# Performance work log

Measured on AMD Instinct MI355X. Metric: run time of the kernel, lower is better.

The kernel has to match this reference:

```python
import jax, jax.numpy as jnp
import numpy as np

B, S, H = 64, 2048, 512


def setup_inputs() -> dict:
    key = jax.random.key(0)
    ks = jax.random.split(key, 7)
    sc = 1.0 / np.sqrt(H)
    return {
        "encoder_outputs": jax.random.normal(ks[0], (B, S, H), dtype=jnp.float32),
        "hidden": jax.random.normal(ks[1], (B, H), dtype=jnp.float32),
        "W1": jax.random.uniform(ks[2], (H, H), jnp.float32, -sc, sc),
        "b1": jax.random.uniform(ks[3], (H,), jnp.float32, -sc, sc),
        "W2": jax.random.uniform(ks[4], (H, H), jnp.float32, -sc, sc),
        "b2": jax.random.uniform(ks[5], (H,), jnp.float32, -sc, sc),
        "V": jax.random.uniform(ks[6], (H, 1), jnp.float32, -sc, sc),
        "bV": jnp.zeros((1,), dtype=jnp.float32),
    }


def reference(encoder_outputs, hidden, W1, b1, W2, b2, V, bV):
    # score: tanh(W1(enc) + W2(hidden)) ; hidden broadcast over seq dim (no repeat materialized)
    proj_enc = jnp.einsum("bsh,hk->bsk", encoder_outputs, W1) + b1          # [B,S,H]
    proj_hid = (hidden @ W2 + b2)[:, None, :]                                 # [B,1,H]
    score = jnp.tanh(proj_enc + proj_hid)                                     # [B,S,H]
    logits = jnp.einsum("bsh,hk->bsk", score, V) + bV                        # [B,S,1]
    attention_weights = jax.nn.softmax(logits, axis=1)                        # softmax over seq
    context = jnp.sum(attention_weights * encoder_outputs, axis=1)            # [B,H]
    return context, attention_weights
```

## Files before the change

### kernel.cpp

```cpp
#include <hip/hip_runtime.h>
#include <hip/hip_bf16.h>
#include <cstdint>
#include <cstddef>

#define B_ 64
#define S_ 2048
#define H_ 512

typedef __bf16 bf16x8 __attribute__((ext_vector_type(8)));
typedef float  f32x4  __attribute__((ext_vector_type(4)));

__device__ __forceinline__ float fast_tanh(float x) {
    float e = __expf(2.0f * x);
    return 1.0f - __fdividef(2.0f, e + 1.0f);
}

__global__ __launch_bounds__(256) void prep_kernel(const float* __restrict__ W1,
                                                   unsigned short* __restrict__ Wt,
                                                   const float* __restrict__ hidden,
                                                   const float* __restrict__ W2,
                                                   const float* __restrict__ b1,
                                                   const float* __restrict__ b2,
                                                   float* __restrict__ cvals) {
    if (blockIdx.x < 256) {
        __shared__ float tile[32][33];
        int tn = blockIdx.x >> 4;
        int tk = blockIdx.x & 15;
        int lx = threadIdx.x & 31;
        int ly = threadIdx.x >> 5;
#pragma unroll
        for (int i = 0; i < 4; ++i) {
            int k = tk * 32 + ly + i * 8;
            tile[ly + i * 8][lx] = W1[k * H_ + tn * 32 + lx];
        }
        __syncthreads();
#pragma unroll
        for (int i = 0; i < 4; ++i) {
            int n = tn * 32 + ly + i * 8;
            float v = tile[lx][ly + i * 8];
            __bf16 bv = (__bf16)v;
            Wt[(size_t)n * H_ + tk * 32 + lx] = *(unsigned short*)&bv;
        }
    } else {
        int blk = blockIdx.x - 256;
        int b = blk >> 1;
        int h = (blk & 1) * 256 + threadIdx.x;
        float acc = b1[h] + b2[h];
        const float* hp = hidden + b * H_;
        const float* wp = W2 + h;
#pragma unroll 16
        for (int k = 0; k < H_; ++k) acc = fmaf(hp[k], wp[(size_t)k * H_], acc);
        cvals[b * H_ + h] = acc;
    }
}

__global__ __launch_bounds__(256, 4) void score_kernel(const float* __restrict__ enc,
                                                       const unsigned short* __restrict__ Wt,
                                                       const float* __restrict__ cvals,
                                                       const float* __restrict__ Vp,
                                                       float* __restrict__ logits) {
    __shared__ __align__(16) unsigned short As[128 * 64];
    __shared__ __align__(16) unsigned short Bs[128 * 64];

    int orig = blockIdx.x;
    int wg   = (orig & 7) * 512 + (orig >> 3);
    int b     = wg >> 6;
    int stile = (wg >> 2) & 15;
    int ntile = wg & 3;

    int tid  = threadIdx.x;
    int wid  = tid >> 6;
    int lane = tid & 63;
    int wm = wid >> 1, wn = wid & 1;
    int rsel = lane & 15;
    int g    = lane >> 4;

    f32x4 acc[4][4];
#pragma unroll
    for (int m = 0; m < 4; ++m)
#pragma unroll
        for (int n = 0; n < 4; ++n) acc[m][n] = (f32x4){0.f, 0.f, 0.f, 0.f};

    const float*          Abase = enc + ((size_t)(b * S_ + stile * 128)) * H_;
    const unsigned short* Bbase = Wt + ((size_t)(ntile * 128)) * H_;

    int srow = tid >> 1;
    int shalf = (tid & 1);
    int c0 = shalf * 2;

    float4 ra[4];
    bf16x8 rb[2];

    auto swz = [&](int row, int nbc) -> int {
        return row * 64 + ((nbc ^ (row & 7)) << 3);
    };

    auto loadAB = [&](int kt) {
        const float* ap = Abase + (size_t)srow * H_ + kt * 32 + shalf * 16;
        ra[0] = *(const float4*)(ap);
        ra[1] = *(const float4*)(ap + 4);
        ra[2] = *(const float4*)(ap + 8);
        ra[3] = *(const float4*)(ap + 12);
        const unsigned short* bp = Bbase + (size_t)srow * H_ + kt * 32 + shalf * 16;
        rb[0] = *(const bf16x8*)(bp);
        rb[1] = *(const bf16x8*)(bp + 8);
    };
    auto writeAB = [&](int nb) {
        bf16x8 va[2];
        const float* f = (const float*)&ra[0];
#pragma unroll
        for (int j = 0; j < 2; ++j)
#pragma unroll
            for (int i = 0; i < 8; ++i) va[j][i] = (__bf16)f[j * 8 + i];
#pragma unroll
        for (int j = 0; j < 2; ++j) {
            int idx = swz(srow, nb * 4 + c0 + j);
            *(bf16x8*)&As[idx] = va[j];
            *(bf16x8*)&Bs[idx] = rb[j];
        }
    };
    auto compute = [&](int cb) {
        bf16x8 af[4], bfr[4];
#pragma unroll
        for (int m = 0; m < 4; ++m) {
            int row = wm * 64 + m * 16 + rsel;
            af[m] = *(const bf16x8*)&As[swz(row, cb * 4 + g)];
        }
#pragma unroll
        for (int n = 0; n < 4; ++n) {
            int row = wn * 64 + n * 16 + rsel;
            bfr[n] = *(const bf16x8*)&Bs[swz(row, cb * 4 + g)];
        }
#pragma unroll
        for (int m = 0; m < 4; ++m)
#pragma unroll
            for (int n = 0; n < 4; ++n)
                acc[m][n] = __builtin_amdgcn_mfma_f32_16x16x32_bf16(
                    af[m], bfr[n], acc[m][n], 0, 0, 0);
    };

    loadAB(0);
    writeAB(0);
    __syncthreads();

    for (int kt = 0; kt < 16; ++kt) {
        int cur = kt & 1;
        if (kt < 15) loadAB(kt + 1);
        compute(cur);
        if (kt < 15) writeAB(cur ^ 1);
        __syncthreads();
    }

    int csel = rsel;
    float cw[4], vv[4];
#pragma unroll
    for (int n = 0; n < 4; ++n) {
        int col = ntile * 128 + wn * 64 + n * 16 + csel;
        cw[n] = cvals[b * H_ + col];
        vv[n] = Vp[col];
    }
    float part[16];
#pragma unroll
    for (int m = 0; m < 4; ++m)
#pragma unroll
        for (int r = 0; r < 4; ++r) {
            float p = 0.f;
#pragma unroll
            for (int n = 0; n < 4; ++n) {
                float s = fast_tanh(acc[m][n][r] + cw[n]);
                p = fmaf(vv[n], s, p);
            }
            part[m * 4 + r] = p;
        }
#pragma unroll
    for (int i = 0; i < 16; ++i)
#pragma unroll
        for (int off = 1; off < 16; off <<= 1)
            part[i] += __shfl_xor(part[i], off);

    if (csel == 0) {
        int gq = lane >> 4;
#pragma unroll
        for (int m = 0; m < 4; ++m)
#pragma unroll
            for (int r = 0; r < 4; ++r) {
                int row = stile * 128 + wm * 64 + m * 16 + gq * 4 + r;
                atomicAdd(&logits[b * S_ + row], part[m * 4 + r]);
            }
    }
}

__global__ __launch_bounds__(256) void softmax_kernel(const float* __restrict__ logits,
                                                      float* __restrict__ wout) {
    int b = blockIdx.x;
    int t = threadIdx.x;
    __shared__ float red[8];
    float v[8];
#pragma unroll
    for (int i = 0; i < 8; ++i) v[i] = logits[b * S_ + t + i * 256];
    float m = v[0];
#pragma unroll
    for (int i = 1; i < 8; ++i) m = fmaxf(m, v[i]);
#pragma unroll
    for (int off = 32; off >= 1; off >>= 1) m = fmaxf(m, __shfl_xor(m, off));
    int wid = t >> 6, lane = t & 63;
    if (lane == 0) red[wid] = m;
    __syncthreads();
    m = fmaxf(fmaxf(red[0], red[1]), fmaxf(red[2], red[3]));
    float s = 0.f;
#pragma unroll
    for (int i = 0; i < 8; ++i) { v[i] = __expf(v[i] - m); s += v[i]; }
#pragma unroll
    for (int off = 32; off >= 1; off >>= 1) s += __shfl_xor(s, off);
    if (lane == 0) red[4 + wid] = s;
    __syncthreads();
    float tot = red[4] + red[5] + red[6] + red[7];
    float inv = __fdividef(1.0f, tot);
#pragma unroll
    for (int i = 0; i < 8; ++i) wout[b * S_ + t + i * 256] = v[i] * inv;
}

__global__ __launch_bounds__(512) void context_kernel(const float* __restrict__ enc,
                                                      const float* __restrict__ w,
                                                      float* __restrict__ ctx) {
    int b  = blockIdx.x >> 4;
    int sc = blockIdx.x & 15;
    int h  = threadIdx.x;
    const float* ep = enc + ((size_t)(b * S_ + sc * 128)) * H_ + h;
    const float* wp = w + b * S_ + sc * 128;
    float acc = 0.f;
#pragma unroll 8
    for (int i = 0; i < 128; ++i) acc = fmaf(wp[i], ep[(size_t)i * H_], acc);
    atomicAdd(&ctx[b * H_ + h], acc);
}

extern "C" void kernel_launch(void* const* d_in, const int* in_sizes, int n_in,
                              void* d_out, int out_size, void* d_ws, size_t ws_size,
                              hipStream_t stream) {
    (void)in_sizes; (void)n_in; (void)out_size; (void)ws_size;
    const float* enc    = (const float*)d_in[0];
    const float* hidden = (const float*)d_in[1];
    const float* W1     = (const float*)d_in[2];
    const float* b1     = (const float*)d_in[3];
    const float* W2     = (const float*)d_in[4];
    const float* b2     = (const float*)d_in[5];
    const float* Vp     = (const float*)d_in[6];

    char* ws = (char*)d_ws;
    unsigned short* Wt = (unsigned short*)ws;
    float* cvals  = (float*)(ws + 524288);
    float* logits = (float*)(ws + 524288 + 131072);

    float* ctx  = (float*)d_out;
    float* wout = ctx + B_ * H_;

    hipMemsetAsync(logits, 0, (size_t)B_ * S_ * sizeof(float), stream);
    hipMemsetAsync(ctx,    0, (size_t)B_ * H_ * sizeof(float), stream);

    prep_kernel<<<384, 256, 0, stream>>>(W1, Wt, hidden, W2, b1, b2, cvals);
    score_kernel<<<4096, 256, 0, stream>>>(enc, Wt, cvals, Vp, logits);
    softmax_kernel<<<64, 256, 0, stream>>>(logits, wout);
    context_kernel<<<1024, 512, 0, stream>>>(enc, wout, ctx);
}
```

Measured before the change: 551.5 us.

## Pre-convert encoder to bf16 and use async LDS-load double-buffered score GEMM

Adds a conversion pass that writes the fp32 encoder outputs as bf16 into workspace. A new score kernel then streams bf16 A and B tiles straight into LDS with global_load_lds, double-buffered across the K loop, and feeds MFMA. This removes the per-tile fp32-to-bf16 conversion inside the GEMM and halves the bytes the score kernel re-reads across its four N tiles. In exchange it adds a full extra pass over the encoder tensor and a 128MB workspace, and it only runs when the workspace is large enough.

New measurement: 606.2 us. +9.9%, slower.

```diff
diff --git a/kernel.cpp b/kernel.cpp
--- a/kernel.cpp
+++ b/kernel.cpp
@@ -10,9 +10,27 @@
 typedef __bf16 bf16x8 __attribute__((ext_vector_type(8)));
 typedef float  f32x4  __attribute__((ext_vector_type(4)));
 
+#define AS_GLB __attribute__((address_space(1)))
+#define AS_LDS __attribute__((address_space(3)))
+
 __device__ __forceinline__ float fast_tanh(float x) {
     float e = __expf(2.0f * x);
     return 1.0f - __fdividef(2.0f, e + 1.0f);
+}
+
+__global__ __launch_bounds__(256) void conv_kernel(const float* __restrict__ enc,
+                                                   unsigned short* __restrict__ encb) {
+    size_t base = ((size_t)blockIdx.x * 256 + threadIdx.x) * 8;
+#pragma unroll
+    for (int it = 0; it < 8; ++it) {
+        size_t idx = base + (size_t)it * 8388608;
+        float4 a = *(const float4*)(enc + idx);
+        float4 c = *(const float4*)(enc + idx + 4);
+        bf16x8 v;
+        v[0] = (__bf16)a.x; v[1] = (__bf16)a.y; v[2] = (__bf16)a.z; v[3] = (__bf16)a.w;
+        v[4] = (__bf16)c.x; v[5] = (__bf16)c.y; v[6] = (__bf16)c.z; v[7] = (__bf16)c.w;
+        *(bf16x8*)(encb + idx) = v;
+    }
 }
 
 __global__ __launch_bounds__(256) void prep_kernel(const float* __restrict__ W1,
@@ -54,6 +72,121 @@
     }
 }
 
+__global__ __launch_bounds__(256) void score97_kernel(const unsigned short* __restrict__ encb,
+                                                      const unsigned short* __restrict__ Wt,
+                                                      const float* __restrict__ cvals,
+                                                      const float* __restrict__ Vp,
+                                                      float* __restrict__ logits) {
+    __shared__ __align__(16) unsigned short As[2][128][64];
+    __shared__ __align__(16) unsigned short Bs[2][128][64];
+
+    int orig = blockIdx.x;
+    int wg   = (orig & 7) * 512 + (orig >> 3);
+    int b     = wg >> 6;
+    int stile = (wg >> 2) & 15;
+    int ntile = wg & 3;
+
+    int tid  = threadIdx.x;
+    int wid  = tid >> 6;
+    int lane = tid & 63;
+    int wm = wid >> 1, wn = wid & 1;
+    int rsel = lane & 15;
+    int g    = lane >> 4;
+
+    f32x4 acc[4][4];
+#pragma unroll
+    for (int m = 0; m < 4; ++m)
+#pragma unroll
+        for (int n = 0; n < 4; ++n) acc[m][n] = (f32x4){0.f, 0.f, 0.f, 0.f};
+
+    const unsigned short* Abase = encb + ((size_t)(b * S_ + stile * 128)) * H_;
+    const unsigned short* Bbase = Wt + ((size_t)(ntile * 128)) * H_;
+
+    int lrow = lane >> 3;
+    int lcol = (lane & 7) * 8;
+
+    auto stage = [&](int nb, int kt) {
+        int kk = kt * 64;
+#pragma unroll
+        for (int i = 0; i < 4; ++i) {
+            int chunk = wid * 4 + i;
+            int row = chunk * 8 + lrow;
+            __builtin_amdgcn_global_load_lds(
+                (const AS_GLB unsigned int*)(Abase + (size_t)row * H_ + kk + lcol),
+                (AS_LDS unsigned int*)&As[nb][chunk * 8][0], 16, 0, 0);
+            __builtin_amdgcn_global_load_lds(
+                (const AS_GLB unsigned int*)(Bbase + (size_t)row * H_ + kk + lcol),
+                (AS_LDS unsigned int*)&Bs[nb][chunk * 8][0], 16, 0, 0);
+        }
+    };
+    auto compute = [&](int cb) {
+#pragma unroll
+        for (int ks = 0; ks < 2; ++ks) {
+            int kof = ks * 32 + g * 8;
+            bf16x8 af[4], bfr[4];
+#pragma unroll
+            for (int m = 0; m < 4; ++m)
+                af[m] = *(const bf16x8*)&As[cb][wm * 64 + m * 16 + rsel][kof];
+#pragma unroll
+            for (int n = 0; n < 4; ++n)
+                bfr[n] = *(const bf16x8*)&Bs[cb][wn * 64 + n * 16 + rsel][kof];
+#pragma unroll
+            for (int m = 0; m < 4; ++m)
+#pragma unroll
+                for (int n = 0; n < 4; ++n)
+                    acc[m][n] = __builtin_amdgcn_mfma_f32_16x16x32_bf16(
+                        af[m], bfr[n], acc[m][n], 0, 0, 0);
+        }
+    };
+
+    stage(0, 0);
+    __syncthreads();
+    for (int kt = 0; kt < 8; ++kt) {
+        int cur = kt & 1;
+        if (kt < 7) stage(cur ^ 1, kt + 1);
+        compute(cur);
+        __syncthreads();
+    }
+
+    int csel = rsel;
+    float cw[4], vv[4];
+#pragma unroll
+    for (int n = 0; n < 4; ++n) {
+        int col = ntile * 128 + wn * 64 + n * 16 + csel;
+        cw[n] = cvals[b * H_ + col];
+        vv[n] = Vp[col];
+    }
+    float part[16];
+#pragma unroll
+    for (int m = 0; m < 4; ++m)
+#pragma unroll
+        for (int r = 0; r < 4; ++r) {
+            float p = 0.f;
+#pragma unroll
+            for (int n = 0; n < 4; ++n) {
+                float s = fast_tanh(acc[m][n][r] + cw[n]);
+                p = fmaf(vv[n], s, p);
+            }
+            part[m * 4 + r] = p;
+        }
+#pragma unroll
+    for (int i = 0; i < 16; ++i)
+#pragma unroll
+        for (int off = 1; off < 16; off <<= 1)
+            part[i] += __shfl_xor(part[i], off);
+
+    if (csel == 0) {
+        int gq = lane >> 4;
+#pragma unroll
+        for (int m = 0; m < 4; ++m)
+#pragma unroll
+            for (int r = 0; r < 4; ++r) {
+                int row = stile * 128 + wm * 64 + m * 16 + gq * 4 + r;
+                atomicAdd(&logits[b * S_ + row], part[m * 4 + r]);
+            }
+    }
+}
+
 __global__ __launch_bounds__(256, 4) void score_kernel(const float* __restrict__ enc,
                                                        const unsigned short* __restrict__ Wt,
                                                        const float* __restrict__ cvals,
@@ -237,7 +370,7 @@
 extern "C" void kernel_launch(void* const* d_in, const int* in_sizes, int n_in,
                               void* d_out, int out_size, void* d_ws, size_t ws_size,
                               hipStream_t stream) {
-    (void)in_sizes; (void)n_in; (void)out_size; (void)ws_size;
+    (void)in_sizes; (void)n_in; (void)out_size;
     const float* enc    = (const float*)d_in[0];
     const float* hidden = (const float*)d_in[1];
     const float* W1     = (const float*)d_in[2];
@@ -250,6 +383,10 @@
     unsigned short* Wt = (unsigned short*)ws;
     float* cvals  = (float*)(ws + 524288);
     float* logits = (float*)(ws + 524288 + 131072);
+    unsigned short* encb = (unsigned short*)(ws + 2097152);
+
+    const size_t need = 2097152 + (size_t)B_ * S_ * H_ * 2;
+    const bool big = ws_size >= need;
 
     float* ctx  = (float*)d_out;
     float* wout = ctx + B_ * H_;
@@ -258,7 +395,12 @@
     hipMemsetAsync(ctx,    0, (size_t)B_ * H_ * sizeof(float), stream);
 
     prep_kernel<<<384, 256, 0, stream>>>(W1, Wt, hidden, W2, b1, b2, cvals);
-    score_kernel<<<4096, 256, 0, stream>>>(enc, Wt, cvals, Vp, logits);
+    if (big) {
+        conv_kernel<<<4096, 256, 0, stream>>>(enc, encb);
+        score97_kernel<<<4096, 256, 0, stream>>>(encb, Wt, cvals, Vp, logits);
+    } else {
+        score_kernel<<<4096, 256, 0, stream>>>(enc, Wt, cvals, Vp, logits);
+    }
     softmax_kernel<<<64, 256, 0, stream>>>(logits, wout);
     context_kernel<<<1024, 512, 0, stream>>>(enc, wout, ctx);
 }
```

## Stage score GEMM tiles via direct global-to-LDS loads and split context work finer

Applied to the files above, without the earlier changes.

The score GEMM no longer stages tiles through registers. It issues global_load_lds to copy fp32 encoder tiles (XOR-swizzled) and bf16 weight tiles straight into double-buffered LDS, and does the fp32-to-bf16 conversion when fragments are read for the MFMA. This removes the register round trip and frees VGPRs. In exchange the LDS footprint for A grows (fp32), the occupancy hint drops to 3, and the conversion work is repeated for every fragment read. Separately, the context kernel now processes 64 sequence rows per block instead of 128, doubling the grid for more parallelism at the cost of twice as many atomics.

New measurement: 566.1 us. +2.6%, slower.

```diff
diff --git a/kernel.cpp b/kernel.cpp
--- a/kernel.cpp
+++ b/kernel.cpp
@@ -9,6 +9,9 @@
 
 typedef __bf16 bf16x8 __attribute__((ext_vector_type(8)));
 typedef float  f32x4  __attribute__((ext_vector_type(4)));
+
+#define AS_GLB __attribute__((address_space(1)))
+#define AS_LDS __attribute__((address_space(3)))
 
 __device__ __forceinline__ float fast_tanh(float x) {
     float e = __expf(2.0f * x);
@@ -54,13 +57,13 @@
     }
 }
 
-__global__ __launch_bounds__(256, 4) void score_kernel(const float* __restrict__ enc,
-                                                       const unsigned short* __restrict__ Wt,
-                                                       const float* __restrict__ cvals,
-                                                       const float* __restrict__ Vp,
-                                                       float* __restrict__ logits) {
-    __shared__ __align__(16) unsigned short As[128 * 64];
-    __shared__ __align__(16) unsigned short Bs[128 * 64];
+__global__ __launch_bounds__(256, 3) void score97b_kernel(const float* __restrict__ enc,
+                                                          const unsigned short* __restrict__ Wt,
+                                                          const float* __restrict__ cvals,
+                                                          const float* __restrict__ Vp,
+                                                          float* __restrict__ logits) {
+    __shared__ __align__(16) float          Asf[2][128][32];
+    __shared__ __align__(16) unsigned short Bsh[2][128][32];
 
     int orig = blockIdx.x;
     int wg   = (orig & 7) * 512 + (orig >> 3);
@@ -84,52 +87,48 @@
     const float*          Abase = enc + ((size_t)(b * S_ + stile * 128)) * H_;
     const unsigned short* Bbase = Wt + ((size_t)(ntile * 128)) * H_;
 
-    int srow = tid >> 1;
-    int shalf = (tid & 1);
-    int c0 = shalf * 2;
-
-    float4 ra[4];
-    bf16x8 rb[2];
-
-    auto swz = [&](int row, int nbc) -> int {
-        return row * 64 + ((nbc ^ (row & 7)) << 3);
+    int arow0 = (lane >> 3);
+    int ac    = lane & 7;
+    int brow0 = (lane >> 2);
+    int bc    = lane & 3;
+
+    auto stage = [&](int nb, int kt) {
+#pragma unroll
+        for (int i = 0; i < 4; ++i) {
+            int row = i * 32 + wid * 8 + arow0;
+            const float* src = Abase + (size_t)row * H_ + kt * 32 + ((ac ^ (row & 7)) << 2);
+            __builtin_amdgcn_global_load_lds((const AS_GLB unsigned int*)src,
+                                             (AS_LDS unsigned int*)&Asf[nb][i * 32 + wid * 8][0],
+                                             16, 0, 0);
+        }
+#pragma unroll
+        for (int i = 0; i < 2; ++i) {
+            int row = i * 64 + wid * 16 + brow0;
+            const unsigned short* src = Bbase + (size_t)row * H_ + kt * 32 + bc * 8;
+            __builtin_amdgcn_global_load_lds((const AS_GLB unsigned int*)src,
+                                             (AS_LDS unsigned int*)&Bsh[nb][i * 64 + wid * 16][0],
+                                             16, 0, 0);
+        }
     };
 
-    auto loadAB = [&](int kt) {
-        const float* ap = Abase + (size_t)srow * H_ + kt * 32 + shalf * 16;
-        ra[0] = *(const float4*)(ap);
-        ra[1] = *(const float4*)(ap + 4);
-        ra[2] = *(const float4*)(ap + 8);
-        ra[3] = *(const float4*)(ap + 12);
-        const unsigned short* bp = Bbase + (size_t)srow * H_ + kt * 32 + shalf * 16;
-        rb[0] = *(const bf16x8*)(bp);
-        rb[1] = *(const bf16x8*)(bp + 8);
-    };
-    auto writeAB = [&](int nb) {
-        bf16x8 va[2];
-        const float* f = (const float*)&ra[0];
-#pragma unroll
-        for (int j = 0; j < 2; ++j)
-#pragma unroll
-            for (int i = 0; i < 8; ++i) va[j][i] = (__bf16)f[j * 8 + i];
-#pragma unroll
-        for (int j = 0; j < 2; ++j) {
-            int idx = swz(srow, nb * 4 + c0 + j);
-            *(bf16x8*)&As[idx] = va[j];
-            *(bf16x8*)&Bs[idx] = rb[j];
-        }
-    };
     auto compute = [&](int cb) {
         bf16x8 af[4], bfr[4];
 #pragma unroll
         for (int m = 0; m < 4; ++m) {
             int row = wm * 64 + m * 16 + rsel;
-            af[m] = *(const bf16x8*)&As[swz(row, cb * 4 + g)];
+            int r7  = row & 7;
+            f32x4 lo = *(const f32x4*)&Asf[cb][row][((2 * g) ^ r7) << 2];
+            f32x4 hi = *(const f32x4*)&Asf[cb][row][((2 * g + 1) ^ r7) << 2];
+#pragma unroll
+            for (int j = 0; j < 4; ++j) {
+                af[m][j]     = (__bf16)lo[j];
+                af[m][4 + j] = (__bf16)hi[j];
+            }
         }
 #pragma unroll
         for (int n = 0; n < 4; ++n) {
             int row = wn * 64 + n * 16 + rsel;
-            bfr[n] = *(const bf16x8*)&Bs[swz(row, cb * 4 + g)];
+            bfr[n] = *(const bf16x8*)&Bsh[cb][row][g * 8];
         }
 #pragma unroll
         for (int m = 0; m < 4; ++m)
@@ -139,15 +138,12 @@
                     af[m], bfr[n], acc[m][n], 0, 0, 0);
     };
 
-    loadAB(0);
-    writeAB(0);
+    stage(0, 0);
     __syncthreads();
-
     for (int kt = 0; kt < 16; ++kt) {
         int cur = kt & 1;
-        if (kt < 15) loadAB(kt + 1);
+        if (kt < 15) stage(cur ^ 1, kt + 1);
         compute(cur);
-        if (kt < 15) writeAB(cur ^ 1);
         __syncthreads();
     }
 
@@ -223,14 +219,14 @@
 __global__ __launch_bounds__(512) void context_kernel(const float* __restrict__ enc,
                                                       const float* __restrict__ w,
                                                       float* __restrict__ ctx) {
-    int b  = blockIdx.x >> 4;
-    int sc = blockIdx.x & 15;
+    int b  = blockIdx.x >> 5;
+    int sc = blockIdx.x & 31;
     int h  = threadIdx.x;
-    const float* ep = enc + ((size_t)(b * S_ + sc * 128)) * H_ + h;
-    const float* wp = w + b * S_ + sc * 128;
+    const float* ep = enc + ((size_t)(b * S_ + sc * 64)) * H_ + h;
+    const float* wp = w + b * S_ + sc * 64;
     float acc = 0.f;
 #pragma unroll 8
-    for (int i = 0; i < 128; ++i) acc = fmaf(wp[i], ep[(size_t)i * H_], acc);
+    for (int i = 0; i < 64; ++i) acc = fmaf(wp[i], ep[(size_t)i * H_], acc);
     atomicAdd(&ctx[b * H_ + h], acc);
 }
 
@@ -258,7 +254,7 @@
     hipMemsetAsync(ctx,    0, (size_t)B_ * H_ * sizeof(float), stream);
 
     prep_kernel<<<384, 256, 0, stream>>>(W1, Wt, hidden, W2, b1, b2, cvals);
-    score_kernel<<<4096, 256, 0, stream>>>(enc, Wt, cvals, Vp, logits);
+    score97b_kernel<<<4096, 256, 0, stream>>>(enc, Wt, cvals, Vp, logits);
     softmax_kernel<<<64, 256, 0, stream>>>(logits, wout);
-    context_kernel<<<1024, 512, 0, stream>>>(enc, wout, ctx);
-}
+    context_kernel<<<2048, 512, 0, stream>>>(enc, wout, ctx);
+}
```
